# Performance work log

Measured on AMD Instinct MI355X. Metric: run time of the kernel, lower is better.

The kernel has to match this reference:

```python
import jax, jax.numpy as jnp
import numpy as np

N_PTS = 65536
N_VERTS = 6890
N_JOINTS = 24


def build_rotation(q):
    # q: [N,4] unnormalized quaternion (r, x, y, z) -> [N,3,3] rotation matrix
    q = q / jnp.linalg.norm(q, axis=-1, keepdims=True)
    r, x, y, z = q[:, 0], q[:, 1], q[:, 2], q[:, 3]
    R = jnp.stack([
        1 - 2 * (y * y + z * z), 2 * (x * y - r * z), 2 * (x * z + r * y),
        2 * (x * y + r * z), 1 - 2 * (x * x + z * z), 2 * (y * z - r * x),
        2 * (x * z - r * y), 2 * (y * z + r * x), 1 - 2 * (x * x + y * y),
    ], axis=-1).reshape(-1, 3, 3)
    return R


def setup_inputs() -> dict:
    key = jax.random.key(0)
    k1, k2, k3, k4, k5 = jax.random.split(key, 5)
    xyz = jax.random.normal(k1, (N_PTS, 3), dtype=jnp.float32)
    rotation = jax.random.normal(k2, (N_PTS, 4), dtype=jnp.float32)
    smpl_verts = jax.random.normal(k3, (N_VERTS, 3), dtype=jnp.float32)
    skinning_weights = jax.random.uniform(k4, (N_VERTS, N_JOINTS), dtype=jnp.float32)
    # row-normalize like real LBS weights
    skinning_weights = skinning_weights / jnp.sum(skinning_weights, axis=-1, keepdims=True)
    bone_transforms = jax.random.normal(k5, (N_JOINTS, 4, 4), dtype=jnp.float32)
    return {"xyz": xyz, "rotation": rotation, "smpl_verts": smpl_verts,
            "skinning_weights": skinning_weights, "bone_transforms": bone_transforms}


def reference(xyz, rotation, smpl_verts, skinning_weights, bone_transforms):
    # --- 1-NN brute-force search (knn_points with K=1) ---
    d2 = (jnp.sum(xyz * xyz, axis=-1, keepdims=True)
          - 2.0 * (xyz @ smpl_verts.T)
          + jnp.sum(smpl_verts * smpl_verts, axis=-1)[None, :])
    p_idx = jnp.argmin(d2, axis=-1)                      # [N]

    # --- skinning-weight gather ---
    pts_W = skinning_weights[p_idx]                      # [N, 24]

    # --- LBS: blend bone transforms ---
    T_fwd = (pts_W @ bone_transforms.reshape(-1, 16)).reshape(-1, 4, 4)  # [N,4,4]

    # --- transform points (homogeneous) ---
    x_bar = jnp.einsum('nij,nj->ni', T_fwd[:, :3, :3], xyz) + T_fwd[:, :3, 3]  # [N,3]

    # --- rotate covariance rotations ---
    rotation_hat = build_rotation(rotation)              # [N,3,3]
    rotation_bar = jnp.einsum('nij,njk->nik', T_fwd[:, :3, :3], rotation_hat)  # [N,3,3]

    return (x_bar, rotation_bar, T_fwd)
```

## Files before the change

### kernel.cpp

```cpp
#include <hip/hip_runtime.h>
#include <math.h>

#define NPTS 65536
#define NV 6890
#define NT 432
#define NTPAD 8
#define VSPLIT 4
#define TILES_PER_WAVE (NT / VSPLIT)
#define NJ 24
#define PTS_PER_BLK 64
#define NBLK (NPTS / PTS_PER_BLK)

typedef double f64x4 __attribute__((ext_vector_type(4)));

__global__ void prep_frags_k(const float* __restrict__ verts, double* __restrict__ bf) {
    int e = blockIdx.x * blockDim.x + threadIdx.x;
    if (e >= (NT + NTPAD) * 64) return;
    int l = e & 63;
    int t = e >> 6;
    int j = t * 16 + (l & 15);
    int k = l >> 4;
    double val;
    if (j < NV) {
        if (k < 3) {
            val = (double)verts[3 * j + k];
        } else {
            double x = (double)verts[3 * j + 0];
            double y = (double)verts[3 * j + 1];
            double z = (double)verts[3 * j + 2];
            val = x * x + y * y + z * z;
        }
    } else {
        val = (k == 3) ? 1e300 : 0.0;
    }
    bf[e] = val;
}

__device__ __forceinline__ double packdx(double d, unsigned orv) {
    unsigned long long u = __double_as_longlong(d);
    u = (u & ~0x1FFFULL) | (unsigned long long)orv;
    return __longlong_as_double(u);
}

__launch_bounds__(256)
__global__ void smplnn_main(const float* __restrict__ xyz,
                            const float* __restrict__ rot,
                            const double* __restrict__ bf,
                            const float* __restrict__ sw,
                            const float* __restrict__ bt,
                            float* __restrict__ out) {
    __shared__ double smin[VSPLIT][4][16][16];

    const int tid  = threadIdx.x;
    const int lane = tid & 63;
    const int wave = tid >> 6;
    const int r = lane & 15;
    const int k = lane >> 4;
    const int pbase = blockIdx.x * PTS_PER_BLK;

    double a0 = (k == 3) ? 1.0 : -2.0 * (double)xyz[3 * (pbase +      r) + k];
    double a1 = (k == 3) ? 1.0 : -2.0 * (double)xyz[3 * (pbase + 16 + r) + k];
    double a2 = (k == 3) ? 1.0 : -2.0 * (double)xyz[3 * (pbase + 32 + r) + k];
    double a3 = (k == 3) ? 1.0 : -2.0 * (double)xyz[3 * (pbase + 48 + r) + k];

    const f64x4 zero = {0.0, 0.0, 0.0, 0.0};

    double ar  = (k == 3) ? (double)r : 0.0;
    double one = (k == 3) ? 1.0 : 0.0;
    f64x4 drow = __builtin_amdgcn_mfma_f64_16x16x4f64(ar, one, zero, 0, 0, 0);
    f64x4 dcol = __builtin_amdgcn_mfma_f64_16x16x4f64(one, ar, zero, 0, 0, 0);
    int rowid[4];
    unsigned colb[4];
    #pragma unroll
    for (int v = 0; v < 4; ++v) { rowid[v] = (int)drow[v]; colb[v] = (unsigned)(int)dcol[v]; }

    double m0[4], m1[4], m2[4], m3[4];
    #pragma unroll
    for (int v = 0; v < 4; ++v) { m0[v] = 1e301; m1[v] = 1e301; m2[v] = 1e301; m3[v] = 1e301; }

    const int tbase = wave * TILES_PER_WAVE;
    const double* bl = bf + (size_t)tbase * 64 + lane;
    double b0 = bl[0];
    double b1 = bl[64];
    for (int t = 0; t < TILES_PER_WAVE; t += 2) {
        double p0 = bl[(size_t)(t + 2) * 64];
        double p1 = bl[(size_t)(t + 3) * 64];
        {
            const unsigned tb = (unsigned)((tbase + t) << 4);
            f64x4 d0 = __builtin_amdgcn_mfma_f64_16x16x4f64(a0, b0, zero, 0, 0, 0);
            f64x4 d1 = __builtin_amdgcn_mfma_f64_16x16x4f64(a1, b0, zero, 0, 0, 0);
            f64x4 d2 = __builtin_amdgcn_mfma_f64_16x16x4f64(a2, b0, zero, 0, 0, 0);
            f64x4 d3 = __builtin_amdgcn_mfma_f64_16x16x4f64(a3, b0, zero, 0, 0, 0);
            #pragma unroll
            for (int v = 0; v < 4; ++v) {
                const unsigned orv = tb | colb[v];
                m0[v] = fmin(m0[v], packdx(d0[v], orv));
                m1[v] = fmin(m1[v], packdx(d1[v], orv));
                m2[v] = fmin(m2[v], packdx(d2[v], orv));
                m3[v] = fmin(m3[v], packdx(d3[v], orv));
            }
        }
        {
            const unsigned tb = (unsigned)((tbase + t + 1) << 4);
            f64x4 d0 = __builtin_amdgcn_mfma_f64_16x16x4f64(a0, b1, zero, 0, 0, 0);
            f64x4 d1 = __builtin_amdgcn_mfma_f64_16x16x4f64(a1, b1, zero, 0, 0, 0);
            f64x4 d2 = __builtin_amdgcn_mfma_f64_16x16x4f64(a2, b1, zero, 0, 0, 0);
            f64x4 d3 = __builtin_amdgcn_mfma_f64_16x16x4f64(a3, b1, zero, 0, 0, 0);
            #pragma unroll
            for (int v = 0; v < 4; ++v) {
                const unsigned orv = tb | colb[v];
                m0[v] = fmin(m0[v], packdx(d0[v], orv));
                m1[v] = fmin(m1[v], packdx(d1[v], orv));
                m2[v] = fmin(m2[v], packdx(d2[v], orv));
                m3[v] = fmin(m3[v], packdx(d3[v], orv));
            }
        }
        b0 = p0;
        b1 = p1;
    }

    #pragma unroll
    for (int v = 0; v < 4; ++v) {
        smin[wave][0][rowid[v]][colb[v]] = m0[v];
        smin[wave][1][rowid[v]][colb[v]] = m1[v];
        smin[wave][2][rowid[v]][colb[v]] = m2[v];
        smin[wave][3][rowid[v]][colb[v]] = m3[v];
    }
    __syncthreads();

    if (wave != 0) return;
    const int set = lane >> 4;
    const int row = lane & 15;
    const int i = pbase + lane;

    double best = 1e302;
    #pragma unroll
    for (int w = 0; w < VSPLIT; ++w) {
        #pragma unroll
        for (int c = 0; c < 16; ++c) {
            best = fmin(best, smin[w][set][row][c]);
        }
    }
    const int bi = (int)(__double_as_longlong(best) & 0x1FFFULL);

    const float xf = xyz[3 * i + 0];
    const float yf = xyz[3 * i + 1];
    const float zf = xyz[3 * i + 2];

    const float* W = &sw[bi * NJ];
    float Tm[16];
    #pragma unroll
    for (int q = 0; q < 16; ++q) Tm[q] = 0.0f;
    #pragma unroll
    for (int kk = 0; kk < NJ; ++kk) {
        float w = W[kk];
        #pragma unroll
        for (int q = 0; q < 16; ++q) Tm[q] = fmaf(w, bt[16 * kk + q], Tm[q]);
    }

    float xb0 = Tm[0] * xf + Tm[1] * yf + Tm[2]  * zf + Tm[3];
    float xb1 = Tm[4] * xf + Tm[5] * yf + Tm[6]  * zf + Tm[7];
    float xb2 = Tm[8] * xf + Tm[9] * yf + Tm[10] * zf + Tm[11];

    float qr = rot[4 * i + 0];
    float qx = rot[4 * i + 1];
    float qy = rot[4 * i + 2];
    float qz = rot[4 * i + 3];
    float inv = 1.0f / sqrtf(qr * qr + qx * qx + qy * qy + qz * qz);
    qr *= inv; qx *= inv; qy *= inv; qz *= inv;

    float Rh[9];
    Rh[0] = 1.0f - 2.0f * (qy * qy + qz * qz);
    Rh[1] = 2.0f * (qx * qy - qr * qz);
    Rh[2] = 2.0f * (qx * qz + qr * qy);
    Rh[3] = 2.0f * (qx * qy + qr * qz);
    Rh[4] = 1.0f - 2.0f * (qx * qx + qz * qz);
    Rh[5] = 2.0f * (qy * qz - qr * qx);
    Rh[6] = 2.0f * (qx * qz - qr * qy);
    Rh[7] = 2.0f * (qy * qz + qr * qx);
    Rh[8] = 1.0f - 2.0f * (qx * qx + qy * qy);

    float RB[9];
    #pragma unroll
    for (int rr = 0; rr < 3; ++rr) {
        #pragma unroll
        for (int cc = 0; cc < 3; ++cc) {
            RB[3 * rr + cc] = Tm[4 * rr + 0] * Rh[cc]
                            + Tm[4 * rr + 1] * Rh[3 + cc]
                            + Tm[4 * rr + 2] * Rh[6 + cc];
        }
    }

    out[3 * i + 0] = xb0;
    out[3 * i + 1] = xb1;
    out[3 * i + 2] = xb2;
    float* ob = out + 3 * NPTS + 9 * i;
    #pragma unroll
    for (int q = 0; q < 9; ++q) ob[q] = RB[q];
    float* ot = out + 12 * NPTS + 16 * i;
    #pragma unroll
    for (int q = 0; q < 16; ++q) ot[q] = Tm[q];
}

extern "C" void kernel_launch(void* const* d_in, const int* in_sizes, int n_in,
                              void* d_out, int out_size, void* d_ws, size_t ws_size,
                              hipStream_t stream) {
    const float* xyz   = (const float*)d_in[0];
    const float* rot   = (const float*)d_in[1];
    const float* verts = (const float*)d_in[2];
    const float* sw    = (const float*)d_in[3];
    const float* bt    = (const float*)d_in[4];
    float* out = (float*)d_out;

    double* bfrag = (double*)d_ws;
    prep_frags_k<<<((NT + NTPAD) * 64 + 255) / 256, 256, 0, stream>>>(verts, bfrag);
    smplnn_main<<<NBLK, 256, 0, stream>>>(xyz, rot, bfrag, sw, bt, out);
}
```

Before: 120.9 us.

## Split vertex search across eight waves and reduce minima with shuffles

Doubles the number of waves per block that split the vertex tiles, so each wave runs half as many MFMA iterations, and raises the block to 512 threads. The per-wave column minima are reduced within 16-lane groups via xor shuffles, so only 64 values per wave go to shared memory instead of a full 16x16 tile set. The 2x-unrolled loop becomes a single-tile loop with one-ahead prefetch. This adds more cross-wave reduction work and changes register/occupancy pressure.

```diff
diff --git a/kernel.cpp b/kernel.cpp
--- a/kernel.cpp
+++ b/kernel.cpp
@@ -5,7 +5,7 @@
 #define NV 6890
 #define NT 432
 #define NTPAD 8
-#define VSPLIT 4
+#define VSPLIT 8
 #define TILES_PER_WAVE (NT / VSPLIT)
 #define NJ 24
 #define PTS_PER_BLK 64
@@ -42,14 +42,14 @@
     return __longlong_as_double(u);
 }
 
-__launch_bounds__(256)
+__launch_bounds__(512, 8)
 __global__ void smplnn_main(const float* __restrict__ xyz,
                             const float* __restrict__ rot,
                             const double* __restrict__ bf,
                             const float* __restrict__ sw,
                             const float* __restrict__ bt,
                             float* __restrict__ out) {
-    __shared__ double smin[VSPLIT][4][16][16];
+    __shared__ double smin2[VSPLIT][PTS_PER_BLK];
 
     const int tid  = threadIdx.x;
     const int lane = tid & 63;
@@ -80,67 +80,51 @@
 
     const int tbase = wave * TILES_PER_WAVE;
     const double* bl = bf + (size_t)tbase * 64 + lane;
-    double b0 = bl[0];
-    double b1 = bl[64];
-    for (int t = 0; t < TILES_PER_WAVE; t += 2) {
-        double p0 = bl[(size_t)(t + 2) * 64];
-        double p1 = bl[(size_t)(t + 3) * 64];
-        {
-            const unsigned tb = (unsigned)((tbase + t) << 4);
-            f64x4 d0 = __builtin_amdgcn_mfma_f64_16x16x4f64(a0, b0, zero, 0, 0, 0);
-            f64x4 d1 = __builtin_amdgcn_mfma_f64_16x16x4f64(a1, b0, zero, 0, 0, 0);
-            f64x4 d2 = __builtin_amdgcn_mfma_f64_16x16x4f64(a2, b0, zero, 0, 0, 0);
-            f64x4 d3 = __builtin_amdgcn_mfma_f64_16x16x4f64(a3, b0, zero, 0, 0, 0);
-            #pragma unroll
-            for (int v = 0; v < 4; ++v) {
-                const unsigned orv = tb | colb[v];
-                m0[v] = fmin(m0[v], packdx(d0[v], orv));
-                m1[v] = fmin(m1[v], packdx(d1[v], orv));
-                m2[v] = fmin(m2[v], packdx(d2[v], orv));
-                m3[v] = fmin(m3[v], packdx(d3[v], orv));
-            }
-        }
-        {
-            const unsigned tb = (unsigned)((tbase + t + 1) << 4);
-            f64x4 d0 = __builtin_amdgcn_mfma_f64_16x16x4f64(a0, b1, zero, 0, 0, 0);
-            f64x4 d1 = __builtin_amdgcn_mfma_f64_16x16x4f64(a1, b1, zero, 0, 0, 0);
-            f64x4 d2 = __builtin_amdgcn_mfma_f64_16x16x4f64(a2, b1, zero, 0, 0, 0);
-            f64x4 d3 = __builtin_amdgcn_mfma_f64_16x16x4f64(a3, b1, zero, 0, 0, 0);
-            #pragma unroll
-            for (int v = 0; v < 4; ++v) {
-                const unsigned orv = tb | colb[v];
-                m0[v] = fmin(m0[v], packdx(d0[v], orv));
-                m1[v] = fmin(m1[v], packdx(d1[v], orv));
-                m2[v] = fmin(m2[v], packdx(d2[v], orv));
-                m3[v] = fmin(m3[v], packdx(d3[v], orv));
-            }
-        }
-        b0 = p0;
-        b1 = p1;
-    }
-
-    #pragma unroll
-    for (int v = 0; v < 4; ++v) {
-        smin[wave][0][rowid[v]][colb[v]] = m0[v];
-        smin[wave][1][rowid[v]][colb[v]] = m1[v];
-        smin[wave][2][rowid[v]][colb[v]] = m2[v];
-        smin[wave][3][rowid[v]][colb[v]] = m3[v];
+    double b = bl[0];
+    for (int t = 0; t < TILES_PER_WAVE; ++t) {
+        double p = bl[(size_t)(t + 1) * 64];
+        const unsigned tb = (unsigned)((tbase + t) << 4);
+        f64x4 d0 = __builtin_amdgcn_mfma_f64_16x16x4f64(a0, b, zero, 0, 0, 0);
+        f64x4 d1 = __builtin_amdgcn_mfma_f64_16x16x4f64(a1, b, zero, 0, 0, 0);
+        f64x4 d2 = __builtin_amdgcn_mfma_f64_16x16x4f64(a2, b, zero, 0, 0, 0);
+        f64x4 d3 = __builtin_amdgcn_mfma_f64_16x16x4f64(a3, b, zero, 0, 0, 0);
+        #pragma unroll
+        for (int v = 0; v < 4; ++v) {
+            const unsigned orv = tb | colb[v];
+            m0[v] = fmin(m0[v], packdx(d0[v], orv));
+            m1[v] = fmin(m1[v], packdx(d1[v], orv));
+            m2[v] = fmin(m2[v], packdx(d2[v], orv));
+            m3[v] = fmin(m3[v], packdx(d3[v], orv));
+        }
+        b = p;
+    }
+
+    #pragma unroll
+    for (int s = 1; s < 16; s <<= 1) {
+        #pragma unroll
+        for (int v = 0; v < 4; ++v) {
+            m0[v] = fmin(m0[v], __shfl_xor(m0[v], s, 16));
+            m1[v] = fmin(m1[v], __shfl_xor(m1[v], s, 16));
+            m2[v] = fmin(m2[v], __shfl_xor(m2[v], s, 16));
+            m3[v] = fmin(m3[v], __shfl_xor(m3[v], s, 16));
+        }
+    }
+
+    {
+        const int sub = lane & 15;
+        const int f = sub >> 2;
+        const int v = sub & 3;
+        double val = (f == 0) ? m0[v] : (f == 1) ? m1[v] : (f == 2) ? m2[v] : m3[v];
+        smin2[wave][f * 16 + rowid[v]] = val;
     }
     __syncthreads();
 
     if (wave != 0) return;
-    const int set = lane >> 4;
-    const int row = lane & 15;
     const int i = pbase + lane;
 
-    double best = 1e302;
-    #pragma unroll
-    for (int w = 0; w < VSPLIT; ++w) {
-        #pragma unroll
-        for (int c = 0; c < 16; ++c) {
-            best = fmin(best, smin[w][set][row][c]);
-        }
-    }
+    double best = smin2[0][lane];
+    #pragma unroll
+    for (int w = 1; w < VSPLIT; ++w) best = fmin(best, smin2[w][lane]);
     const int bi = (int)(__double_as_longlong(best) & 0x1FFFULL);
 
     const float xf = xyz[3 * i + 0];
@@ -214,5 +198,5 @@
 
     double* bfrag = (double*)d_ws;
     prep_frags_k<<<((NT + NTPAD) * 64 + 255) / 256, 256, 0, stream>>>(verts, bfrag);
-    smplnn_main<<<NBLK, 256, 0, stream>>>(xyz, rot, bfrag, sw, bt, out);
-}
+    smplnn_main<<<NBLK, 512, 0, stream>>>(xyz, rot, bfrag, sw, bt, out);
+}
```

Measured after the change: 426.1 us. 253% more time.

## Split vertex scan across two grid halves with a separate merge-and-epilogue kernel

Applied to the files above, without the earlier changes.

The vertex range is now split into two halves along a second grid dimension, so twice as many blocks each scan half the tiles and write per-point partial minima to workspace. A new merge kernel combines the two partials and runs the LBS epilogue with all threads active, not just one wave per block. The cross-lane reduction now uses 16-lane xor shuffles instead of a large shared-memory table. In exchange there is an extra launch and a round trip of the partial minima through global memory; a single-pass fallback remains for small workspaces.

```diff
diff --git a/kernel.cpp b/kernel.cpp
--- a/kernel.cpp
+++ b/kernel.cpp
@@ -6,16 +6,16 @@
 #define NT 432
 #define NTPAD 8
 #define VSPLIT 4
-#define TILES_PER_WAVE (NT / VSPLIT)
 #define NJ 24
 #define PTS_PER_BLK 64
 #define NBLK (NPTS / PTS_PER_BLK)
+#define FRAG_DBL ((NT + NTPAD) * 64)
 
 typedef double f64x4 __attribute__((ext_vector_type(4)));
 
 __global__ void prep_frags_k(const float* __restrict__ verts, double* __restrict__ bf) {
     int e = blockIdx.x * blockDim.x + threadIdx.x;
-    if (e >= (NT + NTPAD) * 64) return;
+    if (e >= FRAG_DBL) return;
     int l = e & 63;
     int t = e >> 6;
     int j = t * 16 + (l & 15);
@@ -42,14 +42,82 @@
     return __longlong_as_double(u);
 }
 
+__device__ __forceinline__ void epilogue(int i, int bi,
+                                         const float* __restrict__ xyz,
+                                         const float* __restrict__ rot,
+                                         const float* __restrict__ sw,
+                                         const float* __restrict__ bt,
+                                         float* __restrict__ out) {
+    const float xf = xyz[3 * i + 0];
+    const float yf = xyz[3 * i + 1];
+    const float zf = xyz[3 * i + 2];
+
+    const float* W = &sw[bi * NJ];
+    float Tm[16];
+    #pragma unroll
+    for (int q = 0; q < 16; ++q) Tm[q] = 0.0f;
+    #pragma unroll
+    for (int kk = 0; kk < NJ; ++kk) {
+        float w = W[kk];
+        #pragma unroll
+        for (int q = 0; q < 16; ++q) Tm[q] = fmaf(w, bt[16 * kk + q], Tm[q]);
+    }
+
+    float xb0 = Tm[0] * xf + Tm[1] * yf + Tm[2]  * zf + Tm[3];
+    float xb1 = Tm[4] * xf + Tm[5] * yf + Tm[6]  * zf + Tm[7];
+    float xb2 = Tm[8] * xf + Tm[9] * yf + Tm[10] * zf + Tm[11];
+
+    float qr = rot[4 * i + 0];
+    float qx = rot[4 * i + 1];
+    float qy = rot[4 * i + 2];
+    float qz = rot[4 * i + 3];
+    float inv = 1.0f / sqrtf(qr * qr + qx * qx + qy * qy + qz * qz);
+    qr *= inv; qx *= inv; qy *= inv; qz *= inv;
+
+    float Rh[9];
+    Rh[0] = 1.0f - 2.0f * (qy * qy + qz * qz);
+    Rh[1] = 2.0f * (qx * qy - qr * qz);
+    Rh[2] = 2.0f * (qx * qz + qr * qy);
+    Rh[3] = 2.0f * (qx * qy + qr * qz);
+    Rh[4] = 1.0f - 2.0f * (qx * qx + qz * qz);
+    Rh[5] = 2.0f * (qy * qz - qr * qx);
+    Rh[6] = 2.0f * (qx * qz - qr * qy);
+    Rh[7] = 2.0f * (qy * qz + qr * qx);
+    Rh[8] = 1.0f - 2.0f * (qx * qx + qy * qy);
+
+    float RB[9];
+    #pragma unroll
+    for (int rr = 0; rr < 3; ++rr) {
+        #pragma unroll
+        for (int cc = 0; cc < 3; ++cc) {
+            RB[3 * rr + cc] = Tm[4 * rr + 0] * Rh[cc]
+                            + Tm[4 * rr + 1] * Rh[3 + cc]
+                            + Tm[4 * rr + 2] * Rh[6 + cc];
+        }
+    }
+
+    out[3 * i + 0] = xb0;
+    out[3 * i + 1] = xb1;
+    out[3 * i + 2] = xb2;
+    float* ob = out + 3 * NPTS + 9 * i;
+    #pragma unroll
+    for (int q = 0; q < 9; ++q) ob[q] = RB[q];
+    float* ot = out + 12 * NPTS + 16 * i;
+    #pragma unroll
+    for (int q = 0; q < 16; ++q) ot[q] = Tm[q];
+}
+
+template <int GSPLIT>
 __launch_bounds__(256)
-__global__ void smplnn_main(const float* __restrict__ xyz,
+__global__ void smplnn_scan(const float* __restrict__ xyz,
                             const float* __restrict__ rot,
                             const double* __restrict__ bf,
                             const float* __restrict__ sw,
                             const float* __restrict__ bt,
+                            double* __restrict__ pmin,
                             float* __restrict__ out) {
-    __shared__ double smin[VSPLIT][4][16][16];
+    constexpr int TPW = NT / (VSPLIT * GSPLIT);
+    __shared__ double smin2[VSPLIT][PTS_PER_BLK];
 
     const int tid  = threadIdx.x;
     const int lane = tid & 63;
@@ -78,11 +146,11 @@
     #pragma unroll
     for (int v = 0; v < 4; ++v) { m0[v] = 1e301; m1[v] = 1e301; m2[v] = 1e301; m3[v] = 1e301; }
 
-    const int tbase = wave * TILES_PER_WAVE;
+    const int tbase = (blockIdx.y * VSPLIT + wave) * TPW;
     const double* bl = bf + (size_t)tbase * 64 + lane;
     double b0 = bl[0];
     double b1 = bl[64];
-    for (int t = 0; t < TILES_PER_WAVE; t += 2) {
+    for (int t = 0; t < TPW; t += 2) {
         double p0 = bl[(size_t)(t + 2) * 64];
         double p1 = bl[(size_t)(t + 3) * 64];
         {
@@ -120,86 +188,50 @@
     }
 
     #pragma unroll
-    for (int v = 0; v < 4; ++v) {
-        smin[wave][0][rowid[v]][colb[v]] = m0[v];
-        smin[wave][1][rowid[v]][colb[v]] = m1[v];
-        smin[wave][2][rowid[v]][colb[v]] = m2[v];
-        smin[wave][3][rowid[v]][colb[v]] = m3[v];
+    for (int s = 1; s < 16; s <<= 1) {
+        #pragma unroll
+        for (int v = 0; v < 4; ++v) {
+            m0[v] = fmin(m0[v], __shfl_xor(m0[v], s, 16));
+            m1[v] = fmin(m1[v], __shfl_xor(m1[v], s, 16));
+            m2[v] = fmin(m2[v], __shfl_xor(m2[v], s, 16));
+            m3[v] = fmin(m3[v], __shfl_xor(m3[v], s, 16));
+        }
+    }
+
+    {
+        const int sub = lane & 15;
+        const int f = sub >> 2;
+        const int v = sub & 3;
+        double val = (f == 0) ? m0[v] : (f == 1) ? m1[v] : (f == 2) ? m2[v] : m3[v];
+        smin2[wave][f * 16 + rowid[v]] = val;
     }
     __syncthreads();
 
     if (wave != 0) return;
-    const int set = lane >> 4;
-    const int row = lane & 15;
-    const int i = pbase + lane;
-
-    double best = 1e302;
-    #pragma unroll
-    for (int w = 0; w < VSPLIT; ++w) {
-        #pragma unroll
-        for (int c = 0; c < 16; ++c) {
-            best = fmin(best, smin[w][set][row][c]);
-        }
-    }
+
+    double best = smin2[0][lane];
+    #pragma unroll
+    for (int w = 1; w < VSPLIT; ++w) best = fmin(best, smin2[w][lane]);
+
+    if (GSPLIT > 1) {
+        pmin[blockIdx.y * NPTS + pbase + lane] = best;
+    } else {
+        const int bi = (int)(__double_as_longlong(best) & 0x1FFFULL);
+        epilogue(pbase + lane, bi, xyz, rot, sw, bt, out);
+    }
+}
+
+__launch_bounds__(256)
+__global__ void smplnn_merge(const double* __restrict__ pmin,
+                             const float* __restrict__ xyz,
+                             const float* __restrict__ rot,
+                             const float* __restrict__ sw,
+                             const float* __restrict__ bt,
+                             float* __restrict__ out) {
+    const int i = blockIdx.x * blockDim.x + threadIdx.x;
+    double best = fmin(pmin[i], pmin[NPTS + i]);
     const int bi = (int)(__double_as_longlong(best) & 0x1FFFULL);
-
-    const float xf = xyz[3 * i + 0];
-    const float yf = xyz[3 * i + 1];
-    const float zf = xyz[3 * i + 2];
-
-    const float* W = &sw[bi * NJ];
-    float Tm[16];
-    #pragma unroll
-    for (int q = 0; q < 16; ++q) Tm[q] = 0.0f;
-    #pragma unroll
-    for (int kk = 0; kk < NJ; ++kk) {
-        float w = W[kk];
-        #pragma unroll
-        for (int q = 0; q < 16; ++q) Tm[q] = fmaf(w, bt[16 * kk + q], Tm[q]);
-    }
-
-    float xb0 = Tm[0] * xf + Tm[1] * yf + Tm[2]  * zf + Tm[3];
-    float xb1 = Tm[4] * xf + Tm[5] * yf + Tm[6]  * zf + Tm[7];
-    float xb2 = Tm[8] * xf + Tm[9] * yf + Tm[10] * zf + Tm[11];
-
-    float qr = rot[4 * i + 0];
-    float qx = rot[4 * i + 1];
-    float qy = rot[4 * i + 2];
-    float qz = rot[4 * i + 3];
-    float inv = 1.0f / sqrtf(qr * qr + qx * qx + qy * qy + qz * qz);
-    qr *= inv; qx *= inv; qy *= inv; qz *= inv;
-
-    float Rh[9];
-    Rh[0] = 1.0f - 2.0f * (qy * qy + qz * qz);
-    Rh[1] = 2.0f * (qx * qy - qr * qz);
-    Rh[2] = 2.0f * (qx * qz + qr * qy);
-    Rh[3] = 2.0f * (qx * qy + qr * qz);
-    Rh[4] = 1.0f - 2.0f * (qx * qx + qz * qz);
-    Rh[5] = 2.0f * (qy * qz - qr * qx);
-    Rh[6] = 2.0f * (qx * qz - qr * qy);
-    Rh[7] = 2.0f * (qy * qz + qr * qx);
-    Rh[8] = 1.0f - 2.0f * (qx * qx + qy * qy);
-
-    float RB[9];
-    #pragma unroll
-    for (int rr = 0; rr < 3; ++rr) {
-        #pragma unroll
-        for (int cc = 0; cc < 3; ++cc) {
-            RB[3 * rr + cc] = Tm[4 * rr + 0] * Rh[cc]
-                            + Tm[4 * rr + 1] * Rh[3 + cc]
-                            + Tm[4 * rr + 2] * Rh[6 + cc];
-        }
-    }
-
-    out[3 * i + 0] = xb0;
-    out[3 * i + 1] = xb1;
-    out[3 * i + 2] = xb2;
-    float* ob = out + 3 * NPTS + 9 * i;
-    #pragma unroll
-    for (int q = 0; q < 9; ++q) ob[q] = RB[q];
-    float* ot = out + 12 * NPTS + 16 * i;
-    #pragma unroll
-    for (int q = 0; q < 16; ++q) ot[q] = Tm[q];
+    epilogue(i, bi, xyz, rot, sw, bt, out);
 }
 
 extern "C" void kernel_launch(void* const* d_in, const int* in_sizes, int n_in,
@@ -213,6 +245,16 @@
     float* out = (float*)d_out;
 
     double* bfrag = (double*)d_ws;
-    prep_frags_k<<<((NT + NTPAD) * 64 + 255) / 256, 256, 0, stream>>>(verts, bfrag);
-    smplnn_main<<<NBLK, 256, 0, stream>>>(xyz, rot, bfrag, sw, bt, out);
-}
+    double* pmin  = bfrag + FRAG_DBL;
+
+    prep_frags_k<<<(FRAG_DBL + 255) / 256, 256, 0, stream>>>(verts, bfrag);
+
+    const size_t need = (size_t)FRAG_DBL * 8 + (size_t)2 * NPTS * 8;
+    if (ws_size >= need) {
+        dim3 grid(NBLK, 2);
+        smplnn_scan<2><<<grid, 256, 0, stream>>>(xyz, rot, bfrag, sw, bt, pmin, out);
+        smplnn_merge<<<NPTS / 256, 256, 0, stream>>>(pmin, xyz, rot, sw, bt, out);
+    } else {
+        smplnn_scan<1><<<dim3(NBLK, 1), 256, 0, stream>>>(xyz, rot, bfrag, sw, bt, nullptr, out);
+    }
+}
```

Result: slower. 131.0 us (+8.4%).
